# Kernel optimization log

Measured on AMD Instinct MI355X. Metric: run time of the kernel, lower is better.

Reference implementation:

```python
import jax, jax.numpy as jnp
import numpy as np

B, L, D = 4, 2048, 1024
H, DK, DV = 4, 256, 256
CHUNK = 32
MIN_FLOOR, MAX_FLOOR = 0.01, 0.1
EPS = 1e-5


def _l2norm(x):
    return x * jax.lax.rsqrt(jnp.sum(x * x, -1, keepdims=True) + 1e-6)


def _causal_dwconv(x, w):
    # x: [b, L, C], w: [C, k] -> depthwise causal 1d conv
    b, l, c = x.shape
    k = w.shape[-1]
    xt = jnp.transpose(x, (0, 2, 1))
    y = jax.lax.conv_general_dilated(xt, w[:, None, :], (1,), [(k - 1, 0)],
                                     dimension_numbers=('NCH', 'OIH', 'NCH'),
                                     feature_group_count=c)
    return jnp.transpose(y, (0, 2, 1))


def _delta_rule_chunkwise(q, k, v, beta, chunk=CHUNK):
    # q,k: [b,h,L,dk]; v: [b,h,L,dv]; beta: [b,h,L]; L % chunk == 0
    b, h, l, dk = q.shape
    dv = v.shape[-1]
    q = _l2norm(q)
    k = _l2norm(k)
    v = v * beta[..., None]
    kb = k * beta[..., None]
    n = l // chunk
    resh = lambda t: t.reshape(b, h, n, chunk, t.shape[-1])
    q, k, v, kb = resh(q), resh(k), resh(v), resh(kb)
    tri = jnp.triu(jnp.ones((chunk, chunk), bool))        # incl diag
    strict = jnp.triu(jnp.ones((chunk, chunk), bool), 1)  # excl diag
    att = jnp.where(tri, 0.0, -(kb @ jnp.swapaxes(k, -1, -2)))
    # UT transform: forward substitution building (I - lower)^{-1}
    for i in range(1, chunk):
        upd = jnp.einsum('bhnj,bhnjk->bhnk', att[..., i, :], att)
        att = att.at[..., i, :i].add(upd[..., :i])
    att = att + jnp.eye(chunk, dtype=att.dtype)
    u = att @ v
    w = att @ kb

    def step(S, xs):
        q_i, k_i, u_i, w_i = xs  # [b,h,chunk,d]
        local = jnp.where(strict, 0.0, q_i @ jnp.swapaxes(k_i, -1, -2))
        u_adj = u_i - w_i @ S
        o_i = q_i @ S + local @ u_adj
        return S + jnp.swapaxes(k_i, -1, -2) @ u_adj, o_i

    xs = tuple(jnp.moveaxis(t, 2, 0) for t in (q, k, u, w))
    S0 = jnp.zeros((b, h, dk, dv), q.dtype)
    S, o = jax.lax.scan(step, S0, xs)
    return jnp.moveaxis(o, 0, 2).reshape(b, h, l, dv), S


def _rmsnorm(x, w):
    return x * jax.lax.rsqrt(jnp.mean(x * x, -1, keepdims=True) + EPS) * w


def setup_inputs():
    key = jax.random.key(0)
    ks = jax.random.split(key, 16)
    s = 0.02
    return {
        'hidden_states': jax.random.normal(ks[0], (B, L, D), jnp.float32),
        'W_q': jax.random.normal(ks[1], (D, H * DK), jnp.float32) * s,
        'W_k': jax.random.normal(ks[2], (D, H * DK), jnp.float32) * s,
        'W_v': jax.random.normal(ks[3], (D, H * DV), jnp.float32) * s,
        'W_b': jax.random.normal(ks[4], (D, H), jnp.float32) * s,
        'conv_w_q': jax.random.normal(ks[5], (H * DK, 4), jnp.float32) * 0.3,
        'conv_w_k': jax.random.normal(ks[6], (H * DK, 4), jnp.float32) * 0.3,
        'conv_w_v': jax.random.normal(ks[7], (H * DV, 4), jnp.float32) * 0.3,
        'fir_short_w': jax.random.normal(ks[8], (H, DV, 3), jnp.float32) * 0.1,
        'fir_long_w': jax.random.normal(ks[9], (H, DV, 31), jnp.float32) * 0.1,
        'W_fuse1': jax.random.normal(ks[10], (D + 3 * H * DV, 2 * D), jnp.float32) * s,
        'b_fuse1': jnp.zeros((2 * D,), jnp.float32),
        'W_fuse2': jax.random.normal(ks[11], (2 * D, H * 4), jnp.float32) * s,
        'b_fuse2': jnp.zeros((H * 4,), jnp.float32).at[3::4].set(4.0),
        'others_log_tau': jnp.zeros((H,), jnp.float32),
        'norm_w': jnp.ones((DV,), jnp.float32),
        'W_o': jax.random.normal(ks[12], (H * DV, D), jnp.float32) * s,
    }


def reference(hidden_states, W_q, W_k, W_v, W_b, conv_w_q, conv_w_k, conv_w_v,
              fir_short_w, fir_long_w, W_fuse1, b_fuse1, W_fuse2, b_fuse2,
              others_log_tau, norm_w, W_o):
    b, l, d = hidden_states.shape
    # projections + mandatory short conv (silu activation)
    q = jax.nn.silu(_causal_dwconv(hidden_states @ W_q, conv_w_q))
    k = jax.nn.silu(_causal_dwconv(hidden_states @ W_k, conv_w_k))
    v = jax.nn.silu(_causal_dwconv(hidden_states @ W_v, conv_w_v))
    q = q.reshape(b, l, H, DK)
    k = k.reshape(b, l, H, DK)
    v = v.reshape(b, l, H, DV)
    beta = jax.nn.sigmoid(hidden_states @ W_b)  # [b,l,H]
    delta_out, _ = _delta_rule_chunkwise(
        jnp.transpose(q, (0, 2, 1, 3)), jnp.transpose(k, (0, 2, 1, 3)),
        jnp.transpose(v, (0, 2, 1, 3)), jnp.transpose(beta, (0, 2, 1)))
    delta_out = jnp.transpose(delta_out, (0, 2, 1, 3))  # [b,l,H,DV]
    # depthwise FIR paths on v
    vc = v.reshape(b, l, H * DV)
    fir_s = _causal_dwconv(vc, fir_short_w.reshape(H * DV, -1)).reshape(b, l, H, DV)
    fir_l = _causal_dwconv(vc, fir_long_w.reshape(H * DV, -1)).reshape(b, l, H, DV)
    # fusion gate MLP
    gate_in = jnp.concatenate([hidden_states, fir_s.reshape(b, l, -1),
                               fir_l.reshape(b, l, -1), delta_out.reshape(b, l, -1)], -1)
    hid = jax.nn.gelu(gate_in @ W_fuse1 + b_fuse1, approximate=False)
    logits = (hid @ W_fuse2 + b_fuse2).reshape(b, l, H, 4)
    p_raw = jax.nn.sigmoid(logits[..., 3])
    # token-adaptive context floor
    floor = MIN_FLOOR + (MAX_FLOOR - MIN_FLOOR) * (1.0 - p_raw)
    p_val = (1.0 - floor) * p_raw
    tau = jnp.exp(others_log_tau)  # per-head temperature
    others = jax.nn.softmax(logits[..., :3] / tau[None, None, :, None], -1)
    p_ctx = (1.0 - p_val)[..., None] * others
    o = (p_ctx[..., 0:1] * fir_s + p_ctx[..., 1:2] * fir_l +
         p_ctx[..., 2:3] * delta_out + p_val[..., None] * v)
    o = _rmsnorm(o, norm_w)
    return o.reshape(b, l, H * DV) @ W_o
```

## Files before the change

kernel.cpp:

```cpp
#include <hip/hip_runtime.h>
#include <hip/hip_bf16.h>

#define B_ 4
#define L_ 2048
#define D_ 1024
#define H_ 4
#define DK_ 256
#define DV_ 256
#define NCH 64
#define NTOK 8192

typedef __attribute__((ext_vector_type(8))) short bf16x8;
typedef __attribute__((ext_vector_type(4))) float f32x4;
typedef unsigned int u32;

__device__ __forceinline__ float bu2f(unsigned short u) {
    union { unsigned int i; float f; } x; x.i = ((unsigned int)u) << 16; return x.f;
}
__device__ __forceinline__ unsigned short f2bu(float f) {
    union { __hip_bfloat16 h; unsigned short u; } x; x.h = __float2bfloat16(f); return x.u;
}
#define MFMA16(a, b, c) __builtin_amdgcn_mfma_f32_16x16x32_bf16(a, b, c, 0, 0, 0)

__device__ __forceinline__ void gload16(const void* g, void* l) {
    __builtin_amdgcn_global_load_lds(
        (const __attribute__((address_space(1))) u32*)g,
        (__attribute__((address_space(3))) u32*)l, 16, 0, 0);
}

__global__ __launch_bounds__(256) void k_transpose(const float* __restrict__ in,
                                                   unsigned short* __restrict__ out,
                                                   int K, int N) {
    __shared__ float tile[32][33];
    int k0 = blockIdx.y * 32, n0 = blockIdx.x * 32;
    int tx = threadIdx.x & 31, ty = threadIdx.x >> 5;
#pragma unroll
    for (int r = 0; r < 4; ++r)
        tile[ty + 8 * r][tx] = in[(long)(k0 + ty + 8 * r) * N + n0 + tx];
    __syncthreads();
#pragma unroll
    for (int r = 0; r < 4; ++r)
        out[(long)(n0 + ty + 8 * r) * K + k0 + tx] = f2bu(tile[tx][ty + 8 * r]);
}

__global__ __launch_bounds__(256) void k_padT2(const float* __restrict__ W,
                                               unsigned short* __restrict__ out) {
    long idx = (long)blockIdx.x * 256 + threadIdx.x;
    int n = (int)(idx >> 11), k = (int)(idx & 2047);
    out[idx] = (n < 16) ? f2bu(W[k * 16 + n]) : (unsigned short)0;
}

__global__ __launch_bounds__(256) void k_cvt_hs(const float4* __restrict__ hs4,
                                                unsigned short* __restrict__ gate_in) {
    int idx = blockIdx.x * 256 + threadIdx.x;
    float4 v = hs4[idx];
    int row = idx >> 8;
    int c4 = (idx & 255) * 4;
    ushort4 o;
    o.x = f2bu(v.x); o.y = f2bu(v.y); o.z = f2bu(v.z); o.w = f2bu(v.w);
    *reinterpret_cast<ushort4*>(&gate_in[(long)row * 4096 + c4]) = o;
}

__global__ __launch_bounds__(64) void k_beta(const float* __restrict__ hs,
                                             const float* __restrict__ W_b,
                                             float* __restrict__ beta) {
    int tok = blockIdx.x;
    int lane = threadIdx.x;
    const float* hrow = hs + (long)tok * D_;
    float acc0 = 0, acc1 = 0, acc2 = 0, acc3 = 0;
    for (int c = lane; c < D_; c += 64) {
        float x = hrow[c];
        float4 wb = reinterpret_cast<const float4*>(W_b)[c];
        acc0 += x * wb.x; acc1 += x * wb.y; acc2 += x * wb.z; acc3 += x * wb.w;
    }
#pragma unroll
    for (int off = 32; off; off >>= 1) {
        acc0 += __shfl_down(acc0, off);
        acc1 += __shfl_down(acc1, off);
        acc2 += __shfl_down(acc2, off);
        acc3 += __shfl_down(acc3, off);
    }
    if (lane == 0) {
        int b = tok >> 11, l = tok & 2047;
        beta[((long)(b * H_ + 0)) * L_ + l] = 1.f / (1.f + expf(-acc0));
        beta[((long)(b * H_ + 1)) * L_ + l] = 1.f / (1.f + expf(-acc1));
        beta[((long)(b * H_ + 2)) * L_ + l] = 1.f / (1.f + expf(-acc2));
        beta[((long)(b * H_ + 3)) * L_ + l] = 1.f / (1.f + expf(-acc3));
    }
}

template <int EPI>
__global__ __launch_bounds__(512, 2) void k_gemm256(const unsigned short* __restrict__ A, int lda,
                                                    const unsigned short* __restrict__ BT, int ldb,
                                                    void* __restrict__ Cout, int ldc,
                                                    const float* __restrict__ bias,
                                                    int K, int gx) {
    __shared__ __align__(16) unsigned short As[2][256][64];
    __shared__ __align__(16) unsigned short Bs[2][256][64];
    const int tid = threadIdx.x;
    const int wave = tid >> 6, lane = tid & 63;
    const int lr = lane & 15, lg = lane >> 4;
    const int sl = lane >> 3;
    const int sg = ((lane & 7) ^ (sl & 7)) * 8;
    const int nwg = gridDim.x, cpx = nwg >> 3, orig = blockIdx.x;
    const int wg = (orig & 7) * cpx + (orig >> 3);
    const int m0 = (wg / gx) * 256, n0 = (wg % gx) * 256;
    const unsigned short* Abase = A + (long)(m0 + wave * 8 + sl) * lda + sg;
    const unsigned short* Bbase = BT + (long)(n0 + wave * 8 + sl) * ldb + sg;
    f32x4 acc[16][2] = {};
    const int NT = K >> 6;

#define STG_A(h, nb, k0s) { \
    gload16(Abase + (long)((h) * 128) * lda + (k0s), &As[nb][(h) * 128 + wave * 8][0]); \
    gload16(Abase + (long)((h) * 128 + 64) * lda + (k0s), &As[nb][(h) * 128 + 64 + wave * 8][0]); }
#define STG_B(h, nb, k0s) { \
    gload16(Bbase + (long)((h) * 128) * ldb + (k0s), &Bs[nb][(h) * 128 + wave * 8][0]); \
    gload16(Bbase + (long)((h) * 128 + 64) * ldb + (k0s), &Bs[nb][(h) * 128 + 64 + wave * 8][0]); }
#define LDA_F(dst, mt, ks) dst = *reinterpret_cast<const bf16x8*>( \
    &As[sb][(mt) * 16 + lr][(((ks) * 4 + lg) ^ (lr & 7)) * 8]);
#define LDB_F(dst, nt, ks) dst = *reinterpret_cast<const bf16x8*>( \
    &Bs[sb][wave * 32 + (nt) * 16 + lr][(((ks) * 4 + lg) ^ (lr & 7)) * 8]);
#define BARRIER() { asm volatile("" ::: "memory"); __builtin_amdgcn_s_barrier(); \
                    asm volatile("" ::: "memory"); }
#define DO_MFMA(p) { \
    __builtin_amdgcn_s_setprio(1); \
    _Pragma("unroll") for (int i = 0; i < 4; ++i) \
        _Pragma("unroll") for (int nt = 0; nt < 2; ++nt) { \
            acc[(p) * 4 + i][nt] = MFMA16(a[i][0], bfr[nt][0], acc[(p) * 4 + i][nt]); \
            acc[(p) * 4 + i][nt] = MFMA16(a[i][1], bfr[nt][1], acc[(p) * 4 + i][nt]); } \
    __builtin_amdgcn_s_setprio(0); }

    STG_B(0, 0, 0) STG_B(1, 0, 0) STG_A(0, 0, 0) STG_A(1, 0, 0)
    asm volatile("s_waitcnt vmcnt(2)" ::: "memory");
    BARRIER()

    bf16x8 bfr[2][2];
    for (int t = 0; t < NT; ++t) {
        const int sb = t & 1, nb = sb ^ 1;
        const int k0s = (t + 1) << 6;
        const bool more = (t + 1) < NT;
        {
            if (more) STG_B(0, nb, k0s)
            bf16x8 a[4][2];
            LDB_F(bfr[0][0], 0, 0) LDB_F(bfr[0][1], 0, 1)
            LDB_F(bfr[1][0], 1, 0) LDB_F(bfr[1][1], 1, 1)
#pragma unroll
            for (int i = 0; i < 4; ++i) { LDA_F(a[i][0], 0 * 4 + i, 0) LDA_F(a[i][1], 0 * 4 + i, 1) }
            BARRIER()
            DO_MFMA(0)
            BARRIER()
        }
        {
            if (more) STG_B(1, nb, k0s)
            bf16x8 a[4][2];
#pragma unroll
            for (int i = 0; i < 4; ++i) { LDA_F(a[i][0], 1 * 4 + i, 0) LDA_F(a[i][1], 1 * 4 + i, 1) }
            if (more) { asm volatile("s_waitcnt vmcnt(4)" ::: "memory"); }
            else      { asm volatile("s_waitcnt vmcnt(0)" ::: "memory"); }
            BARRIER()
            DO_MFMA(1)
            BARRIER()
        }
        {
            if (more) STG_A(0, nb, k0s)
            bf16x8 a[4][2];
#pragma unroll
            for (int i = 0; i < 4; ++i) { LDA_F(a[i][0], 2 * 4 + i, 0) LDA_F(a[i][1], 2 * 4 + i, 1) }
            BARRIER()
            DO_MFMA(2)
            BARRIER()
        }
        {
            if (more) STG_A(1, nb, k0s)
            bf16x8 a[4][2];
#pragma unroll
            for (int i = 0; i < 4; ++i) { LDA_F(a[i][0], 3 * 4 + i, 0) LDA_F(a[i][1], 3 * 4 + i, 1) }
            if (more) { asm volatile("s_waitcnt vmcnt(2)" ::: "memory"); }
            else      { asm volatile("s_waitcnt vmcnt(0)" ::: "memory"); }
            BARRIER()
            DO_MFMA(3)
            BARRIER()
        }
    }
#undef STG_A
#undef STG_B
#undef LDA_F
#undef LDB_F
#undef BARRIER
#undef DO_MFMA
#pragma unroll
    for (int mt = 0; mt < 16; ++mt)
#pragma unroll
        for (int nt = 0; nt < 2; ++nt)
#pragma unroll
            for (int r = 0; r < 4; ++r) {
                int row = m0 + mt * 16 + lg * 4 + r;
                int col = n0 + wave * 32 + nt * 16 + lr;
                float v = acc[mt][nt][r];
                if (EPI == 2) {
                    v += bias[col];
                    v = 0.5f * v * (1.f + erff(v * 0.70710678118f));
                }
                if (EPI == 0)
                    reinterpret_cast<float*>(Cout)[(long)row * ldc + col] = v;
                else
                    reinterpret_cast<unsigned short*>(Cout)[(long)row * ldc + col] = f2bu(v);
            }
}

template <int EPI>
__global__ __launch_bounds__(256) void k_gemm(const unsigned short* __restrict__ A, int lda,
                                              const unsigned short* __restrict__ BT, int ldb,
                                              void* __restrict__ Cout, int ldc,
                                              const float* __restrict__ bias,
                                              int K, int gx) {
    __shared__ __align__(16) unsigned short As[128][64];
    __shared__ __align__(16) unsigned short Bs[128][64];
    const int tid = threadIdx.x;
    const int wave = tid >> 6, lane = tid & 63;
    const int wm = wave & 1, wn = wave >> 1;
    const int lr = lane & 15, lg = lane >> 4;
    const int nwg = gridDim.x;
    const int cpx = nwg >> 3;
    const int orig = blockIdx.x;
    const int wg = (orig & 7) * cpx + (orig >> 3);
    const int m0 = (wg / gx) * 128, n0 = (wg % gx) * 128;
    const int srow = wave * 32 + (lane >> 3);
    const int scol = (((lane & 7) ^ ((lane >> 3) & 7))) * 8;
    const unsigned short* Ap = &A[(long)(m0 + srow) * lda + scol];
    const unsigned short* Bp = &BT[(long)(n0 + srow) * ldb + scol];
    unsigned short* AsB = &As[wave * 32][0];
    unsigned short* BsB = &Bs[wave * 32][0];
    const unsigned short* AsF = &As[0][0];
    const unsigned short* BsF = &Bs[0][0];
    f32x4 acc[4][4] = {};
    for (int k0 = 0; k0 < K; k0 += 64) {
#pragma unroll
        for (int g = 0; g < 4; ++g) {
            gload16(Ap + (long)g * 8 * lda + k0, AsB + g * 8 * 64);
            gload16(Bp + (long)g * 8 * ldb + k0, BsB + g * 8 * 64);
        }
        __syncthreads();
#pragma unroll
        for (int ks = 0; ks < 2; ++ks) {
            bf16x8 af[4], bfr[4];
#pragma unroll
            for (int mt = 0; mt < 4; ++mt) {
                int r = wm * 64 + mt * 16 + lr;
                af[mt] = *reinterpret_cast<const bf16x8*>(
                    AsF + r * 64 + (((ks * 4 + lg) ^ (lr & 7)) * 8));
            }
#pragma unroll
            for (int nt = 0; nt < 4; ++nt) {
                int r = wn * 64 + nt * 16 + lr;
                bfr[nt] = *reinterpret_cast<const bf16x8*>(
                    BsF + r * 64 + (((ks * 4 + lg) ^ (lr & 7)) * 8));
            }
#pragma unroll
            for (int mt = 0; mt < 4; ++mt)
#pragma unroll
                for (int nt = 0; nt < 4; ++nt)
                    acc[mt][nt] = MFMA16(af[mt], bfr[nt], acc[mt][nt]);
        }
        __syncthreads();
    }
#pragma unroll
    for (int mt = 0; mt < 4; ++mt)
#pragma unroll
        for (int nt = 0; nt < 4; ++nt)
#pragma unroll
            for (int r = 0; r < 4; ++r) {
                int row = m0 + wm * 64 + mt * 16 + lg * 4 + r;
                int col = n0 + wn * 64 + nt * 16 + lr;
                float v = acc[mt][nt][r];
                if (EPI == 2) {
                    v += bias[col];
                    v = 0.5f * v * (1.f + erff(v * 0.70710678118f));
                }
                if (EPI == 0)
                    reinterpret_cast<float*>(Cout)[(long)row * ldc + col] = v;
                else
                    reinterpret_cast<unsigned short*>(Cout)[(long)row * ldc + col] = f2bu(v);
            }
}

__global__ __launch_bounds__(256) void k_conv_silu(const unsigned short* __restrict__ QKVp,
                                                   const float* __restrict__ cwq,
                                                   const float* __restrict__ cwk,
                                                   const float* __restrict__ cwv,
                                                   unsigned short* __restrict__ qn,
                                                   unsigned short* __restrict__ kn,
                                                   unsigned short* __restrict__ v_blc) {
    int tok = blockIdx.x;
    int b = tok >> 11, l = tok & 2047;
    int t = threadIdx.x;
    float y[12];
#pragma unroll
    for (int j = 0; j < 12; ++j) {
        int c = t + 256 * j;
        const float* cw = (j < 4) ? &cwq[c * 4] : (j < 8) ? &cwk[(c - 1024) * 4] : &cwv[(c - 2048) * 4];
        float s = 0.f;
#pragma unroll
        for (int jj = 0; jj < 4; ++jj) {
            int tl = l - 3 + jj;
            if (tl >= 0) s += bu2f(QKVp[((long)(b * L_ + tl)) * 3072 + c]) * cw[jj];
        }
        y[j] = s / (1.f + expf(-s));
    }
    float sq[8];
#pragma unroll
    for (int j = 0; j < 8; ++j) sq[j] = y[j] * y[j];
    int wave = t >> 6, lane = t & 63;
#pragma unroll
    for (int off = 32; off; off >>= 1)
#pragma unroll
        for (int j = 0; j < 8; ++j) sq[j] += __shfl_down(sq[j], off);
    __shared__ float red[4][8];
    if (lane == 0)
#pragma unroll
        for (int j = 0; j < 8; ++j) red[wave][j] = sq[j];
    __syncthreads();
    float tot[8];
#pragma unroll
    for (int j = 0; j < 8; ++j) tot[j] = red[0][j] + red[1][j] + red[2][j] + red[3][j];
#pragma unroll
    for (int h = 0; h < 4; ++h) {
        float sc = rsqrtf(tot[h] + 1e-6f);
        qn[((long)(b * H_ + h) * L_ + l) * 256 + t] = f2bu(y[h] * sc);
    }
#pragma unroll
    for (int h = 0; h < 4; ++h) {
        float sc = rsqrtf(tot[4 + h] + 1e-6f);
        kn[((long)(b * H_ + h) * L_ + l) * 256 + t] = f2bu(y[4 + h] * sc);
    }
#pragma unroll
    for (int h = 0; h < 4; ++h)
        v_blc[(long)tok * 1024 + h * 256 + t] = f2bu(y[8 + h]);
}

__global__ __launch_bounds__(256) void k_delta_chunk(const unsigned short* __restrict__ qn,
                                                     const unsigned short* __restrict__ kn,
                                                     const unsigned short* __restrict__ v_blc,
                                                     const float* __restrict__ beta,
                                                     unsigned short* __restrict__ u_buf,
                                                     unsigned short* __restrict__ w_buf,
                                                     unsigned short* __restrict__ local_buf,
                                                     unsigned short* __restrict__ kT_buf) {
    int bid = blockIdx.x;
    int n = bid & 63, bh = bid >> 6;
    int b = bh >> 2, h = bh & 3;
    int t0 = n * 32;
    __shared__ __align__(16) unsigned short k_s[32][264];
    __shared__ __align__(16) unsigned short vbT[256][40];
    __shared__ __align__(16) unsigned short kbT[256][40];
    __shared__ __align__(16) float att[32][33];
    __shared__ __align__(16) unsigned short att_b[32][40];
    __shared__ float bet[32];
    int tid = threadIdx.x, wave = tid >> 6, lane = tid & 63;
    int lr = lane & 15, lg = lane >> 4;

    {
        int row = tid >> 3;
        int cc = (tid & 7) * 32;
        float brow = beta[(long)bh * L_ + t0 + row];
        if ((tid & 7) == 0) bet[row] = brow;
        const uint4* kp = reinterpret_cast<const uint4*>(&kn[((long)bh * L_ + t0 + row) * 256 + cc]);
        const uint4* vp = reinterpret_cast<const uint4*>(&v_blc[((long)(b * L_ + t0 + row)) * 1024 + h * 256 + cc]);
        unsigned short kv[32], vv[32];
#pragma unroll
        for (int g = 0; g < 4; ++g) {
            uint4 x = kp[g];
            *reinterpret_cast<uint4*>(&kv[g * 8]) = x;
            *reinterpret_cast<uint4*>(&k_s[row][cc + g * 8]) = x;
            *reinterpret_cast<uint4*>(&vv[g * 8]) = vp[g];
        }
#pragma unroll
        for (int e = 0; e < 32; ++e) {
            kbT[cc + e][row] = f2bu(bu2f(kv[e]) * brow);
            vbT[cc + e][row] = f2bu(bu2f(vv[e]) * brow);
        }
    }
    __syncthreads();

    {
        unsigned short tmp[32];
#pragma unroll
        for (int t = 0; t < 32; ++t) tmp[t] = k_s[t][tid];
#pragma unroll
        for (int g = 0; g < 4; ++g)
            *reinterpret_cast<uint4*>(&kT_buf[((long)bid * 256 + tid) * 32 + g * 8]) =
                *reinterpret_cast<uint4*>(&tmp[g * 8]);
    }

    {
        int i0 = (wave & 1) * 16, j0 = (wave >> 1) * 16;
        f32x4 G = {0, 0, 0, 0}, S2 = {0, 0, 0, 0};
#pragma unroll
        for (int kk = 0; kk < 8; ++kk) {
            bf16x8 bk = *reinterpret_cast<const bf16x8*>(&k_s[j0 + lr][kk * 32 + lg * 8]);
            bf16x8 ak = *reinterpret_cast<const bf16x8*>(&k_s[i0 + lr][kk * 32 + lg * 8]);
            bf16x8 aq = *reinterpret_cast<const bf16x8*>(&qn[((long)bh * L_ + t0 + i0 + lr) * 256 + kk * 32 + lg * 8]);
            G = MFMA16(ak, bk, G);
            S2 = MFMA16(aq, bk, S2);
        }
#pragma unroll
        for (int r = 0; r < 4; ++r) {
            int i = i0 + lg * 4 + r, j = j0 + lr;
            att[i][j] = (j < i) ? -bet[i] * G[r] : 0.f;
            local_buf[(long)bid * 1024 + i * 32 + j] = f2bu((j <= i) ? S2[r] : 0.f);
        }
    }
    __syncthreads();

    for (int i = 1; i < 32; ++i) {
        float upd = 0.f;
        if (tid < i) {
            for (int j = tid + 1; j < i; ++j) upd += att[i][j] * att[j][tid];
        }
        __syncthreads();
        if (tid < i) att[i][tid] += upd;
        __syncthreads();
    }
    for (int e = tid; e < 1024; e += 256) {
        int i = e >> 5, j = e & 31;
        att_b[i][j] = f2bu(att[i][j] + ((i == j) ? 1.f : 0.f));
    }
    __syncthreads();

    {
        int mt = wave & 1;
        bf16x8 afr = *reinterpret_cast<const bf16x8*>(&att_b[mt * 16 + lr][lg * 8]);
        f32x4 z = {0, 0, 0, 0};
#pragma unroll
        for (int ntt = 0; ntt < 8; ++ntt) {
            int n0c = (wave >> 1) * 128 + ntt * 16;
            bf16x8 bu = *reinterpret_cast<const bf16x8*>(&vbT[n0c + lr][lg * 8]);
            bf16x8 bw = *reinterpret_cast<const bf16x8*>(&kbT[n0c + lr][lg * 8]);
            f32x4 ut = MFMA16(afr, bu, z);
            f32x4 wt = MFMA16(afr, bw, z);
#pragma unroll
            for (int r = 0; r < 4; ++r) {
                int t = mt * 16 + lg * 4 + r, c = n0c + lr;
                u_buf[((long)bid * 32 + t) * 256 + c] = f2bu(ut[r]);
                w_buf[((long)bid * 32 + t) * 256 + c] = f2bu(wt[r]);
            }
        }
    }
}

__global__ __launch_bounds__(256) void k_scan(const unsigned short* __restrict__ qn,
                                              const unsigned short* __restrict__ u_buf,
                                              const unsigned short* __restrict__ w_buf,
                                              const unsigned short* __restrict__ local_buf,
                                              const unsigned short* __restrict__ kT_buf,
                                              unsigned short* __restrict__ gate_in) {
    int bid = blockIdx.x;
    int bh = bid & 15, dvb = bid >> 4;
    int b = bh >> 2, h = bh & 3;
    int dc0 = dvb * 16;
    __shared__ __align__(16) unsigned short Tb[16][264];
    __shared__ __align__(16) unsigned short uaT[16][40];
    const int tid = threadIdx.x, wave = tid >> 6, lane = tid & 63;
    const int lr = lane & 15, lg = lane >> 4;
    const int wi = wave & 1;
    const bool isW = wave < 2;
    const int c0w = wave * 64;
    f32x4 Tacc[4] = {};
    for (int e = tid; e < 16 * 264; e += 256) (&Tb[0][0])[e] = 0;
    const unsigned short* q_bh = qn + (long)bh * L_ * 256;
    const unsigned short* u_bh = u_buf + (long)bh * 64 * 8192;
    const unsigned short* w_bh = w_buf + (long)bh * 64 * 8192;
    const unsigned short* l_bh = local_buf + (long)bh * 64 * 1024;
    const unsigned short* kT_bh = kT_buf + (long)bh * 64 * 8192;
    const unsigned short* wq_base = (isW ? w_bh : q_bh) + (16 * wi + lr) * 256;
    const unsigned short* u_base = u_bh + (16 * wi + lg * 4) * 256 + dc0 + lr;
    const unsigned short* l_base = l_bh + (16 * wi + lr) * 32 + lg * 8;
    const unsigned short* kT_base = kT_bh + (c0w + lr) * 32 + lg * 8;
    bf16x8 wqA[8], kB[4], lA = {};
    float uv[4];
    auto prefetch = [&](int n) {
        long o8 = (long)n * 8192;
#pragma unroll
        for (int kk = 0; kk < 8; ++kk)
            wqA[kk] = *reinterpret_cast<const bf16x8*>(wq_base + o8 + kk * 32 + lg * 8);
#pragma unroll
        for (int cc = 0; cc < 4; ++cc)
            kB[cc] = *reinterpret_cast<const bf16x8*>(kT_base + o8 + cc * 512);
        if (isW) {
#pragma unroll
            for (int r = 0; r < 4; ++r) uv[r] = bu2f(u_base[o8 + r * 256]);
        } else {
            lA = *reinterpret_cast<const bf16x8*>(l_base + (long)n * 1024);
        }
    };
    prefetch(0);
    __syncthreads();
    for (int n = 0; n < 64; ++n) {
        f32x4 P0 = {0, 0, 0, 0}, P1 = {0, 0, 0, 0};
#pragma unroll
        for (int kk = 0; kk < 8; kk += 2) {
            bf16x8 t0 = *reinterpret_cast<const bf16x8*>(&Tb[lr][kk * 32 + lg * 8]);
            bf16x8 t1 = *reinterpret_cast<const bf16x8*>(&Tb[lr][(kk + 1) * 32 + lg * 8]);
            P0 = MFMA16(wqA[kk], t0, P0);
            P1 = MFMA16(wqA[kk + 1], t1, P1);
        }
        f32x4 P;
#pragma unroll
        for (int r = 0; r < 4; ++r) P[r] = P0[r] + P1[r];
        if (isW) {
#pragma unroll
            for (int r = 0; r < 4; ++r)
                uaT[lr][16 * wi + lg * 4 + r] = f2bu(uv[r] - P[r]);
        }
        bf16x8 kBc[4];
#pragma unroll
        for (int cc = 0; cc < 4; ++cc) kBc[cc] = kB[cc];
        bf16x8 lAc = lA;
        if (n + 1 < 64) prefetch(n + 1);
        __syncthreads();
        bf16x8 uaA = *reinterpret_cast<const bf16x8*>(&uaT[lr][lg * 8]);
        if (!isW) {
            f32x4 O = MFMA16(lAc, uaA, P);
#pragma unroll
            for (int r = 0; r < 4; ++r) {
                long row = (long)b * L_ + n * 32 + 16 * wi + lg * 4 + r;
                gate_in[row * 4096 + 3072 + h * 256 + dc0 + lr] = f2bu(O[r]);
            }
        }
#pragma unroll
        for (int cc = 0; cc < 4; ++cc)
            Tacc[cc] = MFMA16(uaA, kBc[cc], Tacc[cc]);
#pragma unroll
        for (int cc = 0; cc < 4; ++cc)
#pragma unroll
            for (int r = 0; r < 4; ++r)
                Tb[lg * 4 + r][c0w + cc * 16 + lr] = f2bu(Tacc[cc][r]);
        __syncthreads();
    }
}

__global__ __launch_bounds__(256) void k_fir(const unsigned short* __restrict__ v_blc,
                                             const float* __restrict__ ws3,
                                             const float* __restrict__ wl31,
                                             unsigned short* __restrict__ gate_in) {
    __shared__ unsigned short xs[94][256];
    int b = blockIdx.y, tt = blockIdx.x * 64, c0 = blockIdx.z * 256;
    int tid = threadIdx.x;
    for (int r = 0; r < 94; ++r) {
        int t = tt - 30 + r;
        xs[r][tid] = (t >= 0) ? v_blc[((long)(b * L_ + t)) * 1024 + c0 + tid] : (unsigned short)0;
    }
    int c = c0 + tid;
    float wl[31], ws[3];
#pragma unroll
    for (int j = 0; j < 31; ++j) wl[j] = wl31[(long)c * 31 + j];
#pragma unroll
    for (int j = 0; j < 3; ++j) ws[j] = ws3[(long)c * 3 + j];
    __syncthreads();
    for (int t = 0; t < 64; ++t) {
        float accl = 0.f, accs = 0.f;
#pragma unroll
        for (int j = 0; j < 31; ++j) accl += bu2f(xs[t + j][tid]) * wl[j];
#pragma unroll
        for (int j = 0; j < 3; ++j) accs += bu2f(xs[t + 28 + j][tid]) * ws[j];
        long row = (long)b * L_ + tt + t;
        gate_in[row * 4096 + 1024 + c] = f2bu(accs);
        gate_in[row * 4096 + 2048 + c] = f2bu(accl);
    }
}

__global__ __launch_bounds__(256) void k_gate(const float* __restrict__ logits_pre,
                                              const float* __restrict__ b_fuse2,
                                              const float* __restrict__ log_tau,
                                              const float* __restrict__ norm_w,
                                              const unsigned short* __restrict__ gate_in,
                                              const unsigned short* __restrict__ v_blc,
                                              unsigned short* __restrict__ o_norm) {
    int tok = blockIdx.x;
    int tid = threadIdx.x;
    __shared__ float lg_s[16];
    __shared__ float red[4][4];
    if (tid < 16) lg_s[tid] = logits_pre[(long)tok * 128 + tid] + b_fuse2[tid];
    __syncthreads();
    float o[4];
#pragma unroll
    for (int h = 0; h < 4; ++h) {
        float l0 = lg_s[h * 4 + 0], l1 = lg_s[h * 4 + 1], l2 = lg_s[h * 4 + 2], l3 = lg_s[h * 4 + 3];
        float praw = 1.f / (1.f + expf(-l3));
        float fl_ = 0.01f + 0.09f * (1.f - praw);
        float pval = (1.f - fl_) * praw;
        float itau = expf(-log_tau[h]);
        float a0 = l0 * itau, a1 = l1 * itau, a2 = l2 * itau;
        float m = fmaxf(a0, fmaxf(a1, a2));
        float e0 = expf(a0 - m), e1 = expf(a1 - m), e2 = expf(a2 - m);
        float inv = (1.f - pval) / (e0 + e1 + e2);
        long base = (long)tok * 4096;
        float fs = bu2f(gate_in[base + 1024 + h * 256 + tid]);
        float flv = bu2f(gate_in[base + 2048 + h * 256 + tid]);
        float dd = bu2f(gate_in[base + 3072 + h * 256 + tid]);
        float vv = bu2f(v_blc[(long)tok * 1024 + h * 256 + tid]);
        o[h] = e0 * inv * fs + e1 * inv * flv + e2 * inv * dd + pval * vv;
    }
    int wave = tid >> 6, lane = tid & 63;
    float s[4];
#pragma unroll
    for (int h = 0; h < 4; ++h) s[h] = o[h] * o[h];
#pragma unroll
    for (int off = 32; off; off >>= 1)
#pragma unroll
        for (int h = 0; h < 4; ++h) s[h] += __shfl_down(s[h], off);
    if (lane == 0)
#pragma unroll
        for (int h = 0; h < 4; ++h) red[wave][h] = s[h];
    __syncthreads();
#pragma unroll
    for (int h = 0; h < 4; ++h) {
        float tot = red[0][h] + red[1][h] + red[2][h] + red[3][h];
        float sc = rsqrtf(tot * (1.f / 256.f) + 1e-5f);
        o_norm[(long)tok * 1024 + h * 256 + tid] = f2bu(o[h] * sc * norm_w[tid]);
    }
}

extern "C" void kernel_launch(void* const* d_in, const int* in_sizes, int n_in,
                              void* d_out, int out_size, void* d_ws, size_t ws_size,
                              hipStream_t stream) {
    const float* hs = (const float*)d_in[0];
    const float* W_q = (const float*)d_in[1];
    const float* W_k = (const float*)d_in[2];
    const float* W_v = (const float*)d_in[3];
    const float* W_b = (const float*)d_in[4];
    const float* cwq = (const float*)d_in[5];
    const float* cwk = (const float*)d_in[6];
    const float* cwv = (const float*)d_in[7];
    const float* fir_s_w = (const float*)d_in[8];
    const float* fir_l_w = (const float*)d_in[9];
    const float* W_f1 = (const float*)d_in[10];
    const float* b_f1 = (const float*)d_in[11];
    const float* W_f2 = (const float*)d_in[12];
    const float* b_f2 = (const float*)d_in[13];
    const float* log_tau = (const float*)d_in[14];
    const float* norm_w = (const float*)d_in[15];
    const float* W_o = (const float*)d_in[16];

    char* ws = (char*)d_ws;
    size_t off = 0;
    auto alloc = [&](size_t bytes) { size_t o = off; off += (bytes + 255) & ~(size_t)255; return o; };
    unsigned short* gate_in = (unsigned short*)(ws + alloc((size_t)NTOK * 4096 * 2));
    unsigned short* QKVp    = (unsigned short*)(ws + alloc((size_t)NTOK * 3072 * 2));
    unsigned short* WqkvT   = (unsigned short*)(ws + alloc((size_t)3072 * 1024 * 2));
    unsigned short* Wf1T    = (unsigned short*)(ws + alloc((size_t)2048 * 4096 * 2));
    unsigned short* WoT     = (unsigned short*)(ws + alloc((size_t)1024 * 1024 * 2));
    unsigned short* Wf2Tp   = (unsigned short*)(ws + alloc((size_t)128 * 2048 * 2));
    float*          beta    = (float*)(ws + alloc((size_t)16 * 2048 * 4));
    unsigned short* qn      = (unsigned short*)(ws + alloc((size_t)16 * 2048 * 256 * 2));
    unsigned short* kn      = (unsigned short*)(ws + alloc((size_t)16 * 2048 * 256 * 2));
    unsigned short* v_blc   = (unsigned short*)(ws + alloc((size_t)NTOK * 1024 * 2));
    unsigned short* u_buf   = (unsigned short*)(ws + alloc((size_t)16 * 64 * 8192 * 2));
    unsigned short* w_buf   = (unsigned short*)(ws + alloc((size_t)16 * 64 * 8192 * 2));
    unsigned short* locb    = (unsigned short*)(ws + alloc((size_t)16 * 64 * 1024 * 2));
    unsigned short* kT_buf  = (unsigned short*)(ws + alloc((size_t)16 * 64 * 8192 * 2));
    float*          logits  = (float*)(ws + alloc((size_t)NTOK * 128 * 4));
    unsigned short* o_norm  = (unsigned short*)(ws + alloc((size_t)NTOK * 1024 * 2));
    unsigned short* hid     = QKVp;

    k_transpose<<<dim3(32, 32), 256, 0, stream>>>(W_q, WqkvT, 1024, 1024);
    k_transpose<<<dim3(32, 32), 256, 0, stream>>>(W_k, WqkvT + (size_t)1024 * 1024, 1024, 1024);
    k_transpose<<<dim3(32, 32), 256, 0, stream>>>(W_v, WqkvT + (size_t)2048 * 1024, 1024, 1024);
    k_transpose<<<dim3(64, 128), 256, 0, stream>>>(W_f1, Wf1T, 4096, 2048);
    k_transpose<<<dim3(32, 32), 256, 0, stream>>>(W_o, WoT, 1024, 1024);
    k_padT2<<<1024, 256, 0, stream>>>(W_f2, Wf2Tp);
    k_cvt_hs<<<8192, 256, 0, stream>>>((const float4*)hs, gate_in);
    k_beta<<<8192, 64, 0, stream>>>(hs, W_b, beta);
    k_gemm256<1><<<32 * 12, 512, 0, stream>>>(gate_in, 4096, WqkvT, 1024, QKVp, 3072, nullptr,
                                              1024, 12);
    k_conv_silu<<<8192, 256, 0, stream>>>(QKVp, cwq, cwk, cwv, qn, kn, v_blc);
    k_delta_chunk<<<1024, 256, 0, stream>>>(qn, kn, v_blc, beta, u_buf, w_buf, locb, kT_buf);
    k_scan<<<256, 256, 0, stream>>>(qn, u_buf, w_buf, locb, kT_buf, gate_in);
    k_fir<<<dim3(32, 4, 4), 256, 0, stream>>>(v_blc, fir_s_w, fir_l_w, gate_in);
    k_gemm256<2><<<32 * 8, 512, 0, stream>>>(gate_in, 4096, Wf1T, 4096, hid, 2048, b_f1,
                                             4096, 8);
    k_gemm<0><<<1 * 64, 256, 0, stream>>>(hid, 2048, Wf2Tp, 2048, logits, 128, nullptr,
                                          2048, 1);
    k_gate<<<8192, 256, 0, stream>>>(logits, b_f2, log_tau, norm_w, gate_in, v_blc, o_norm);
    k_gemm<0><<<8 * 64, 256, 0, stream>>>(o_norm, 1024, WoT, 1024, (float*)d_out, 1024, nullptr,
                                          1024, 8);
}
```

Measured before the change: 794.5 us.

## Retile 256x256 GEMM waves into a 2x4 grid to cut LDS fragment traffic

Each of the 8 waves now owns a 128x64 sub-tile (2x4 wave grid) instead of a 256x32 column strip, so every wave reads half as many A fragments from LDS per k-step for a modest increase in B fragments. The k-loop is rebuilt into four MFMA phases over k-halves with A and B stores for the next buffer issued in two groups and a full vmcnt(0) wait before the last phase. This lowers LDS read volume per MFMA but exposes more global-load latency, since the pipelined partial waits are gone.

```diff
diff --git a/kernel.cpp b/kernel.cpp
--- a/kernel.cpp
+++ b/kernel.cpp
@@ -99,6 +99,7 @@
     __shared__ __align__(16) unsigned short Bs[2][256][64];
     const int tid = threadIdx.x;
     const int wave = tid >> 6, lane = tid & 63;
+    const int wm = wave >> 2, wn = wave & 3;
     const int lr = lane & 15, lg = lane >> 4;
     const int sl = lane >> 3;
     const int sg = ((lane & 7) ^ (sl & 7)) * 8;
@@ -107,7 +108,7 @@
     const int m0 = (wg / gx) * 256, n0 = (wg % gx) * 256;
     const unsigned short* Abase = A + (long)(m0 + wave * 8 + sl) * lda + sg;
     const unsigned short* Bbase = BT + (long)(n0 + wave * 8 + sl) * ldb + sg;
-    f32x4 acc[16][2] = {};
+    f32x4 acc[8][4] = {};
     const int NT = K >> 6;
 
 #define STG_A(h, nb, k0s) { \
@@ -117,70 +118,54 @@
     gload16(Bbase + (long)((h) * 128) * ldb + (k0s), &Bs[nb][(h) * 128 + wave * 8][0]); \
     gload16(Bbase + (long)((h) * 128 + 64) * ldb + (k0s), &Bs[nb][(h) * 128 + 64 + wave * 8][0]); }
 #define LDA_F(dst, mt, ks) dst = *reinterpret_cast<const bf16x8*>( \
-    &As[sb][(mt) * 16 + lr][(((ks) * 4 + lg) ^ (lr & 7)) * 8]);
+    &As[sb][wm * 128 + (mt) * 16 + lr][(((ks) * 4 + lg) ^ (lr & 7)) * 8]);
 #define LDB_F(dst, nt, ks) dst = *reinterpret_cast<const bf16x8*>( \
-    &Bs[sb][wave * 32 + (nt) * 16 + lr][(((ks) * 4 + lg) ^ (lr & 7)) * 8]);
+    &Bs[sb][wn * 64 + (nt) * 16 + lr][(((ks) * 4 + lg) ^ (lr & 7)) * 8]);
 #define BARRIER() { asm volatile("" ::: "memory"); __builtin_amdgcn_s_barrier(); \
                     asm volatile("" ::: "memory"); }
-#define DO_MFMA(p) { \
+#define DO_MFMA(mb) { \
     __builtin_amdgcn_s_setprio(1); \
     _Pragma("unroll") for (int i = 0; i < 4; ++i) \
-        _Pragma("unroll") for (int nt = 0; nt < 2; ++nt) { \
-            acc[(p) * 4 + i][nt] = MFMA16(a[i][0], bfr[nt][0], acc[(p) * 4 + i][nt]); \
-            acc[(p) * 4 + i][nt] = MFMA16(a[i][1], bfr[nt][1], acc[(p) * 4 + i][nt]); } \
+        _Pragma("unroll") for (int nt = 0; nt < 4; ++nt) \
+            acc[(mb) + i][nt] = MFMA16(a[i], bfr[nt], acc[(mb) + i][nt]); \
     __builtin_amdgcn_s_setprio(0); }
 
-    STG_B(0, 0, 0) STG_B(1, 0, 0) STG_A(0, 0, 0) STG_A(1, 0, 0)
-    asm volatile("s_waitcnt vmcnt(2)" ::: "memory");
+    STG_A(0, 0, 0) STG_A(1, 0, 0) STG_B(0, 0, 0) STG_B(1, 0, 0)
+    asm volatile("s_waitcnt vmcnt(0)" ::: "memory");
     BARRIER()
 
-    bf16x8 bfr[2][2];
+    bf16x8 bfr[4], a[4];
     for (int t = 0; t < NT; ++t) {
         const int sb = t & 1, nb = sb ^ 1;
         const int k0s = (t + 1) << 6;
         const bool more = (t + 1) < NT;
-        {
-            if (more) STG_B(0, nb, k0s)
-            bf16x8 a[4][2];
-            LDB_F(bfr[0][0], 0, 0) LDB_F(bfr[0][1], 0, 1)
-            LDB_F(bfr[1][0], 1, 0) LDB_F(bfr[1][1], 1, 1)
-#pragma unroll
-            for (int i = 0; i < 4; ++i) { LDA_F(a[i][0], 0 * 4 + i, 0) LDA_F(a[i][1], 0 * 4 + i, 1) }
-            BARRIER()
-            DO_MFMA(0)
-            BARRIER()
-        }
-        {
-            if (more) STG_B(1, nb, k0s)
-            bf16x8 a[4][2];
-#pragma unroll
-            for (int i = 0; i < 4; ++i) { LDA_F(a[i][0], 1 * 4 + i, 0) LDA_F(a[i][1], 1 * 4 + i, 1) }
-            if (more) { asm volatile("s_waitcnt vmcnt(4)" ::: "memory"); }
-            else      { asm volatile("s_waitcnt vmcnt(0)" ::: "memory"); }
-            BARRIER()
-            DO_MFMA(1)
-            BARRIER()
-        }
-        {
-            if (more) STG_A(0, nb, k0s)
-            bf16x8 a[4][2];
-#pragma unroll
-            for (int i = 0; i < 4; ++i) { LDA_F(a[i][0], 2 * 4 + i, 0) LDA_F(a[i][1], 2 * 4 + i, 1) }
-            BARRIER()
-            DO_MFMA(2)
-            BARRIER()
-        }
-        {
-            if (more) STG_A(1, nb, k0s)
-            bf16x8 a[4][2];
-#pragma unroll
-            for (int i = 0; i < 4; ++i) { LDA_F(a[i][0], 3 * 4 + i, 0) LDA_F(a[i][1], 3 * 4 + i, 1) }
-            if (more) { asm volatile("s_waitcnt vmcnt(2)" ::: "memory"); }
-            else      { asm volatile("s_waitcnt vmcnt(0)" ::: "memory"); }
-            BARRIER()
-            DO_MFMA(3)
-            BARRIER()
-        }
+        if (more) { STG_A(0, nb, k0s) STG_A(1, nb, k0s) }
+#pragma unroll
+        for (int nt = 0; nt < 4; ++nt) LDB_F(bfr[nt], nt, 0)
+#pragma unroll
+        for (int i = 0; i < 4; ++i) LDA_F(a[i], i, 0)
+        BARRIER()
+        DO_MFMA(0)
+        BARRIER()
+        if (more) { STG_B(0, nb, k0s) STG_B(1, nb, k0s) }
+#pragma unroll
+        for (int i = 0; i < 4; ++i) LDA_F(a[i], 4 + i, 0)
+        BARRIER()
+        DO_MFMA(4)
+        BARRIER()
+#pragma unroll
+        for (int nt = 0; nt < 4; ++nt) LDB_F(bfr[nt], nt, 1)
+#pragma unroll
+        for (int i = 0; i < 4; ++i) LDA_F(a[i], i, 1)
+        BARRIER()
+        DO_MFMA(0)
+        BARRIER()
+#pragma unroll
+        for (int i = 0; i < 4; ++i) LDA_F(a[i], 4 + i, 1)
+        asm volatile("s_waitcnt vmcnt(0)" ::: "memory");
+        BARRIER()
+        DO_MFMA(4)
+        BARRIER()
     }
 #undef STG_A
 #undef STG_B
@@ -189,13 +174,13 @@
 #undef BARRIER
 #undef DO_MFMA
 #pragma unroll
-    for (int mt = 0; mt < 16; ++mt)
-#pragma unroll
-        for (int nt = 0; nt < 2; ++nt)
+    for (int mt = 0; mt < 8; ++mt)
+#pragma unroll
+        for (int nt = 0; nt < 4; ++nt)
 #pragma unroll
             for (int r = 0; r < 4; ++r) {
-                int row = m0 + mt * 16 + lg * 4 + r;
-                int col = n0 + wave * 32 + nt * 16 + lr;
+                int row = m0 + wm * 128 + mt * 16 + lg * 4 + r;
+                int col = n0 + wn * 64 + nt * 16 + lr;
                 float v = acc[mt][nt][r];
                 if (EPI == 2) {
                     v += bias[col];
```

Result: slower. 837.7 us (+5.4%).
